# Performance work log

Measured on AMD Instinct MI355X. Metric: run time of the kernel, lower is better.

## Reference

```python
import jax, jax.numpy as jnp
import numpy as np

EMBED_DIM = 1024
NUM_HEADS = 16
NUM_KV_HEADS = 4
HEAD_DIM = 64
GQA_RATIO = NUM_HEADS // NUM_KV_HEADS
SCALE = 1.0 / np.sqrt(HEAD_DIM).astype(np.float32)
B, L = 1, 4096
NUM_SEQS = 8  # 8 packed sequences of length 512


def setup_inputs() -> dict:
    key = jax.random.key(0)
    k1, k2, k3, k4, k5 = jax.random.split(key, 5)
    hidden_states = jax.random.normal(k1, (B, L, EMBED_DIM), dtype=jnp.float32)
    cu_seqlens = (jnp.arange(NUM_SEQS + 1, dtype=jnp.int32) * (L // NUM_SEQS))
    s = 1.0 / np.sqrt(EMBED_DIM)
    Wq = jax.random.normal(k2, (EMBED_DIM, NUM_HEADS * HEAD_DIM), dtype=jnp.float32) * s
    Wk = jax.random.normal(k3, (EMBED_DIM, NUM_KV_HEADS * HEAD_DIM), dtype=jnp.float32) * s
    Wv = jax.random.normal(k4, (EMBED_DIM, NUM_KV_HEADS * HEAD_DIM), dtype=jnp.float32) * s
    Wo = jax.random.normal(k5, (NUM_HEADS * HEAD_DIM, EMBED_DIM), dtype=jnp.float32) * s
    return {"hidden_states": hidden_states, "Wq": Wq, "Wk": Wk, "Wv": Wv, "Wo": Wo,
            "cu_seqlens": cu_seqlens}


def reference(hidden_states, Wq, Wk, Wv, Wo, cu_seqlens):
    b, l, d = hidden_states.shape
    # QKV projections (Linear, no bias)
    q = (hidden_states @ Wq).reshape(b, l, NUM_HEADS, HEAD_DIM)
    k = (hidden_states @ Wk).reshape(b, l, NUM_KV_HEADS, HEAD_DIM)
    v = (hidden_states @ Wv).reshape(b, l, NUM_KV_HEADS, HEAD_DIM)
    # GQA: expand kv heads to num_heads (faithful to module's manual expand)
    k = jnp.repeat(k, GQA_RATIO, axis=2)  # [b, l, H, hd]
    v = jnp.repeat(v, GQA_RATIO, axis=2)
    # [b, H, l, hd]
    q = q.transpose(0, 2, 1, 3)
    k = k.transpose(0, 2, 1, 3)
    v = v.transpose(0, 2, 1, 3)
    # block-diagonal varlen mask from cu_seqlens
    pos = jnp.arange(l, dtype=jnp.int32)
    seq_ids = jnp.searchsorted(cu_seqlens, pos, side='right') - 1  # [l]
    mask = seq_ids[:, None] == seq_ids[None, :]                    # [l, l]
    # dense SDPA with mask
    scores = jnp.einsum('bhqd,bhkd->bhqk', q, k) * SCALE
    scores = jnp.where(mask[None, None], scores, jnp.finfo(scores.dtype).min)
    attn = jax.nn.softmax(scores, axis=-1)
    out = jnp.einsum('bhqk,bhkd->bhqd', attn, v)
    out = out.transpose(0, 2, 1, 3).reshape(b, l, NUM_HEADS * HEAD_DIM)
    return out @ Wo
```

## Files before the change

kernel.cpp:

```cpp
#include <hip/hip_runtime.h>
#include <hip/hip_bf16.h>
#include <stdint.h>
#include <stddef.h>

typedef __attribute__((ext_vector_type(8))) short short8;
typedef __attribute__((ext_vector_type(4))) short short4v;
typedef __attribute__((ext_vector_type(4))) float f32x4;

__device__ inline void store_c(float* p, float v) { *p = v; }
__device__ inline void store_c(__hip_bfloat16* p, float v) { *p = __float2bfloat16(v); }

__device__ __forceinline__ void gld_lds16(const __hip_bfloat16* g, __hip_bfloat16* l)
{
#if __has_builtin(__builtin_amdgcn_global_load_lds)
    __builtin_amdgcn_global_load_lds(
        (const __attribute__((address_space(1))) unsigned int*)g,
        (__attribute__((address_space(3))) unsigned int*)l,
        16, 0, 0);
#else
    *(short8*)((char*)l + (threadIdx.x & 63) * 16) = *(const short8*)g;
#endif
}

__global__ __launch_bounds__(256) void convert_kernel(const float* __restrict__ in,
                                                      __hip_bfloat16* __restrict__ out,
                                                      int n4)
{
    int i = blockIdx.x * blockDim.x + threadIdx.x;
    if (i >= n4) return;
    const f32x4 v = *(const f32x4*)(in + (size_t)i * 4);
    union { __hip_bfloat16 t[4]; short4v s4; } u;
    #pragma unroll
    for (int j = 0; j < 4; ++j) u.t[j] = __float2bfloat16(v[j]);
    *(short4v*)(out + (size_t)i * 4) = u.s4;
}

__global__ __launch_bounds__(256) void transpose_kernel(const float* __restrict__ Wq,
                                                        const float* __restrict__ Wk,
                                                        const float* __restrict__ Wv,
                                                        const float* __restrict__ Wo,
                                                        __hip_bfloat16* __restrict__ Wt)
{
    __shared__ float tile[32][33];
    const int bk = blockIdx.x;
    const int bn = blockIdx.y;
    const int tx = threadIdx.x & 31;
    const int ty = threadIdx.x >> 5;
    const int n0 = bn * 32;

    const float* src; int ld; int col0;
    if (n0 < 1024)      { src = Wq; ld = 1024; col0 = n0; }
    else if (n0 < 1280) { src = Wk; ld = 256;  col0 = n0 - 1024; }
    else if (n0 < 1536) { src = Wv; ld = 256;  col0 = n0 - 1280; }
    else                { src = Wo; ld = 1024; col0 = n0 - 1536; }

    #pragma unroll
    for (int r = 0; r < 4; ++r) {
        int k = ty + 8 * r;
        tile[k][tx] = src[(size_t)(bk * 32 + k) * ld + col0 + tx];
    }
    __syncthreads();
    #pragma unroll
    for (int r = 0; r < 4; ++r) {
        int nl = ty + 8 * r;
        Wt[(size_t)(n0 + nl) * 1024 + bk * 32 + tx] = __float2bfloat16(tile[tx][nl]);
    }
}

__global__ __launch_bounds__(256) void vt_kernel(const __hip_bfloat16* __restrict__ QKV,
                                                 __hip_bfloat16* __restrict__ Vt)
{
    __shared__ __hip_bfloat16 tile[32][34];
    const int j0 = blockIdx.x * 32;
    const int c0 = blockIdx.y * 32;
    const int tx = threadIdx.x & 31;
    const int ty = threadIdx.x >> 5;

    #pragma unroll
    for (int r = 0; r < 4; ++r) {
        int jl = ty + 8 * r;
        int j = j0 + jl;
        int srcrow = (j & ~63) + (j & 3) * 16 + ((j >> 2) & 15);
        tile[jl][tx] = QKV[(size_t)srcrow * 1536 + 1280 + c0 + tx];
    }
    __syncthreads();
    #pragma unroll
    for (int r = 0; r < 4; ++r) {
        int cl = ty + 8 * r;
        Vt[(size_t)(c0 + cl) * 4096 + j0 + tx] = tile[tx][cl];
    }
}

template <typename CT>
__global__ __launch_bounds__(512) void gemm128_kernel(const __hip_bfloat16* __restrict__ A,
                                                      const __hip_bfloat16* __restrict__ Bt,
                                                      CT* __restrict__ C,
                                                      int M, int N, int K)
{
    __shared__ __align__(16) __hip_bfloat16 As[128 * 64];
    __shared__ __align__(16) __hip_bfloat16 Bs[128 * 64];

    const int tid  = threadIdx.x;
    const int lane = tid & 63;
    const int wave = tid >> 6;
    const int wr = wave >> 2;
    const int wc = wave & 3;
    const int fr = lane & 15;
    const int fg = lane >> 4;

    const __hip_bfloat16* Ab = A  + (size_t)(blockIdx.x * 128) * K;
    const __hip_bfloat16* Bb = Bt + (size_t)(blockIdx.y * 128) * K;

    const int srow8 = lane >> 3;
    const int sslot = (lane & 7) ^ srow8;

    f32x4 acc[4][2];
    const f32x4 z4 = {0.f, 0.f, 0.f, 0.f};
    #pragma unroll
    for (int i = 0; i < 4; ++i)
        #pragma unroll
        for (int j = 0; j < 2; ++j) acc[i][j] = z4;

    for (int k0 = 0; k0 < K; k0 += 64) {
        #pragma unroll
        for (int i = 0; i < 2; ++i) {
            int c = wave * 2 + i;
            gld_lds16(Ab + (size_t)(c * 8 + srow8) * K + k0 + sslot * 8, &As[c * 512]);
        }
        #pragma unroll
        for (int i = 0; i < 2; ++i) {
            int c = wave * 2 + i;
            gld_lds16(Bb + (size_t)(c * 8 + srow8) * K + k0 + sslot * 8, &Bs[c * 512]);
        }
        __syncthreads();

        short8 af[2][4], bfv[2][2];
        #pragma unroll
        for (int kc = 0; kc < 2; ++kc) {
            #pragma unroll
            for (int mf = 0; mf < 4; ++mf) {
                int rr = wr * 64 + mf * 16 + fr;
                af[kc][mf] = *(const short8*)&As[rr * 64 + (((kc * 4 + fg) ^ (fr & 7)) * 8)];
            }
            #pragma unroll
            for (int nf = 0; nf < 2; ++nf) {
                int cc = wc * 32 + nf * 16 + fr;
                bfv[kc][nf] = *(const short8*)&Bs[cc * 64 + (((kc * 4 + fg) ^ (fr & 7)) * 8)];
            }
        }
        #pragma unroll
        for (int kc = 0; kc < 2; ++kc)
            #pragma unroll
            for (int mf = 0; mf < 4; ++mf)
                #pragma unroll
                for (int nf = 0; nf < 2; ++nf)
                    acc[mf][nf] = __builtin_amdgcn_mfma_f32_16x16x32_bf16(af[kc][mf], bfv[kc][nf], acc[mf][nf], 0, 0, 0);
        __syncthreads();
    }

    const int crow = blockIdx.x * 128 + wr * 64;
    const int ccol = blockIdx.y * 128 + wc * 32;
    #pragma unroll
    for (int mf = 0; mf < 4; ++mf)
        #pragma unroll
        for (int nf = 0; nf < 2; ++nf)
            #pragma unroll
            for (int r = 0; r < 4; ++r) {
                int row = crow + mf * 16 + fg * 4 + r;
                int col = ccol + nf * 16 + fr;
                store_c(&C[(size_t)row * N + col], acc[mf][nf][r]);
            }
}

__global__ __launch_bounds__(256) void attn_kernel(const __hip_bfloat16* __restrict__ QKV,
                                                   const __hip_bfloat16* __restrict__ Vt,
                                                   __hip_bfloat16* __restrict__ O)
{
    __shared__ __align__(16) __hip_bfloat16 Ks[64 * 64];
    __shared__ __align__(16) __hip_bfloat16 Vts[64 * 64];
    __shared__ __align__(16) __hip_bfloat16 Ps[4][16][72];

    const int tid  = threadIdx.x;
    const int lane = tid & 63;
    const int wave = tid >> 6;
    const int qt = blockIdx.x;
    const int h  = blockIdx.y;
    const int sq = blockIdx.z;
    const int kvh = h >> 2;

    const int fr = lane & 15;
    const int fg = lane >> 4;
    const int fk = fg * 8;

    const int sr = lane >> 3;
    const int scol = ((lane & 7) ^ sr) * 8;

    const int q0 = sq * 512 + qt * 64 + wave * 16;

    short8 qf[2];
    #pragma unroll
    for (int kc = 0; kc < 2; ++kc)
        qf[kc] = *(const short8*)(QKV + (size_t)(q0 + fr) * 1536 + h * 64 + kc * 32 + fk);

    const f32x4 z4 = {0.f, 0.f, 0.f, 0.f};
    f32x4 acc_o[4];
    #pragma unroll
    for (int b = 0; b < 4; ++b) acc_o[b] = z4;

    float m_run[4], l_run[4];
    #pragma unroll
    for (int r = 0; r < 4; ++r) { m_run[r] = -1e30f; l_run[r] = 0.f; }

    const float cs = 0.125f * 1.44269504088896340736f;

    for (int t = 0; t < 8; ++t) {
        const int kvbase = sq * 512 + t * 64;

        #pragma unroll
        for (int i = wave; i < 8; i += 4) {
            gld_lds16(QKV + (size_t)(kvbase + i * 8 + sr) * 1536 + 1024 + kvh * 64 + scol,
                      &Ks[i * 512]);
            gld_lds16(Vt + (size_t)(kvh * 64 + i * 8 + sr) * 4096 + kvbase + scol,
                      &Vts[i * 512]);
        }
        __syncthreads();

        f32x4 s[4];
        #pragma unroll
        for (int b = 0; b < 4; ++b) s[b] = z4;
        #pragma unroll
        for (int kc = 0; kc < 2; ++kc) {
            #pragma unroll
            for (int nf = 0; nf < 4; ++nf) {
                short8 kf = *(const short8*)&Ks[(nf * 16 + fr) * 64 + (((kc * 4 + fg) ^ (fr & 7)) * 8)];
                s[nf] = __builtin_amdgcn_mfma_f32_16x16x32_bf16(qf[kc], kf, s[nf], 0, 0, 0);
            }
        }

        #pragma unroll
        for (int r = 0; r < 4; ++r) {
            float mx = fmaxf(fmaxf(s[0][r], s[1][r]), fmaxf(s[2][r], s[3][r]));
            #pragma unroll
            for (int off = 1; off < 16; off <<= 1)
                mx = fmaxf(mx, __shfl_xor(mx, off));
            float mnew = fmaxf(m_run[r], mx);
            float f = exp2f((m_run[r] - mnew) * cs);
            m_run[r] = mnew;
            float p0 = exp2f((s[0][r] - mnew) * cs);
            float p1 = exp2f((s[1][r] - mnew) * cs);
            float p2 = exp2f((s[2][r] - mnew) * cs);
            float p3 = exp2f((s[3][r] - mnew) * cs);
            l_run[r] = l_run[r] * f + (p0 + p1 + p2 + p3);
            #pragma unroll
            for (int nf = 0; nf < 4; ++nf)
                acc_o[nf][r] *= f;
            int rl = fg * 4 + r;
            union { __hip_bfloat16 h[4]; short4v s4; } pw;
            pw.h[0] = __float2bfloat16(p0);
            pw.h[1] = __float2bfloat16(p1);
            pw.h[2] = __float2bfloat16(p2);
            pw.h[3] = __float2bfloat16(p3);
            *(short4v*)&Ps[wave][rl][fr * 4] = pw.s4;
        }

        #pragma unroll
        for (int kc = 0; kc < 2; ++kc) {
            short8 pa = *(const short8*)&Ps[wave][fr][kc * 32 + fk];
            #pragma unroll
            for (int nf = 0; nf < 4; ++nf) {
                short8 vf = *(const short8*)&Vts[(nf * 16 + fr) * 64 + (((kc * 4 + fg) ^ (fr & 7)) * 8)];
                acc_o[nf] = __builtin_amdgcn_mfma_f32_16x16x32_bf16(pa, vf, acc_o[nf], 0, 0, 0);
            }
        }
        __syncthreads();
    }

    #pragma unroll
    for (int r = 0; r < 4; ++r) {
        float lsum = l_run[r];
        #pragma unroll
        for (int off = 1; off < 16; off <<= 1)
            lsum += __shfl_xor(lsum, off);
        float inv_l = 1.0f / lsum;
        int row = q0 + fg * 4 + r;
        #pragma unroll
        for (int nf = 0; nf < 4; ++nf)
            O[(size_t)row * 1024 + h * 64 + nf * 16 + fr] =
                __float2bfloat16(acc_o[nf][r] * inv_l);
    }
}

extern "C" void kernel_launch(void* const* d_in, const int* in_sizes, int n_in,
                              void* d_out, int out_size, void* d_ws, size_t ws_size,
                              hipStream_t stream)
{
    const float* hs = (const float*)d_in[0];
    const float* Wq = (const float*)d_in[1];
    const float* Wk = (const float*)d_in[2];
    const float* Wv = (const float*)d_in[3];
    const float* Wo = (const float*)d_in[4];

    char* ws = (char*)d_ws;
    __hip_bfloat16* hsb  = (__hip_bfloat16*)(ws);
    __hip_bfloat16* Wt   = (__hip_bfloat16*)(ws + 8388608);
    __hip_bfloat16* QKV  = (__hip_bfloat16*)(ws + 13631488);
    __hip_bfloat16* AOut = (__hip_bfloat16*)(ws + 26214400);
    __hip_bfloat16* Vt   = (__hip_bfloat16*)(ws + 34603008);
    float* out = (float*)d_out;

    convert_kernel<<<4096, 256, 0, stream>>>(hs, hsb, 1048576);
    transpose_kernel<<<dim3(32, 80), 256, 0, stream>>>(Wq, Wk, Wv, Wo, Wt);
    gemm128_kernel<__hip_bfloat16><<<dim3(32, 12), 512, 0, stream>>>(hsb, Wt, QKV, 4096, 1536, 1024);
    vt_kernel<<<dim3(128, 8), 256, 0, stream>>>(QKV, Vt);
    attn_kernel<<<dim3(8, 16, 8), 256, 0, stream>>>(QKV, Vt, AOut);
    gemm128_kernel<float><<<dim3(32, 8), 512, 0, stream>>>(AOut, Wt + (size_t)1536 * 1024, out, 4096, 1024, 1024);
}
```

Measured before the change: 154.3 us.

## Merge convert and transpose prep kernels; retile GEMMs to 64-row blocks

Merges the fp32->bf16 activation conversion and the weight transpose into one prep kernel launch that branches on block index, saving one launch. Replaces the 128x128, 512-thread GEMM with a 64xBN, 256-thread GEMM templated on BN (192 for the QKV projection, 128 for the output projection). This gives 512 blocks per GEMM instead of 384 and 256, to fill more compute units on the MI355X. In exchange each block reuses less data per tile, so more global and LDS loads are issued per MFMA.

Result: faster. 149.4 us (-3.2%).

```diff
diff --git a/kernel.cpp b/kernel.cpp
--- a/kernel.cpp
+++ b/kernel.cpp
@@ -22,28 +22,28 @@
 #endif
 }
 
-__global__ __launch_bounds__(256) void convert_kernel(const float* __restrict__ in,
-                                                      __hip_bfloat16* __restrict__ out,
-                                                      int n4)
-{
-    int i = blockIdx.x * blockDim.x + threadIdx.x;
-    if (i >= n4) return;
-    const f32x4 v = *(const f32x4*)(in + (size_t)i * 4);
-    union { __hip_bfloat16 t[4]; short4v s4; } u;
-    #pragma unroll
-    for (int j = 0; j < 4; ++j) u.t[j] = __float2bfloat16(v[j]);
-    *(short4v*)(out + (size_t)i * 4) = u.s4;
-}
-
-__global__ __launch_bounds__(256) void transpose_kernel(const float* __restrict__ Wq,
-                                                        const float* __restrict__ Wk,
-                                                        const float* __restrict__ Wv,
-                                                        const float* __restrict__ Wo,
-                                                        __hip_bfloat16* __restrict__ Wt)
+__global__ __launch_bounds__(256) void prep_kernel(const float* __restrict__ hs,
+                                                   const float* __restrict__ Wq,
+                                                   const float* __restrict__ Wk,
+                                                   const float* __restrict__ Wv,
+                                                   const float* __restrict__ Wo,
+                                                   __hip_bfloat16* __restrict__ hsb,
+                                                   __hip_bfloat16* __restrict__ Wt)
 {
     __shared__ float tile[32][33];
-    const int bk = blockIdx.x;
-    const int bn = blockIdx.y;
+    const int b = blockIdx.x;
+    if (b < 4096) {
+        int i = b * 256 + threadIdx.x;
+        const f32x4 v = *(const f32x4*)(hs + (size_t)i * 4);
+        union { __hip_bfloat16 t[4]; short4v s4; } u;
+        #pragma unroll
+        for (int j = 0; j < 4; ++j) u.t[j] = __float2bfloat16(v[j]);
+        *(short4v*)(hsb + (size_t)i * 4) = u.s4;
+        return;
+    }
+    const int bb = b - 4096;
+    const int bk = bb & 31;
+    const int bn = bb >> 5;
     const int tx = threadIdx.x & 31;
     const int ty = threadIdx.x >> 5;
     const int n0 = bn * 32;
@@ -91,79 +91,78 @@
     }
 }
 
-template <typename CT>
-__global__ __launch_bounds__(512) void gemm128_kernel(const __hip_bfloat16* __restrict__ A,
-                                                      const __hip_bfloat16* __restrict__ Bt,
-                                                      CT* __restrict__ C,
-                                                      int M, int N, int K)
-{
-    __shared__ __align__(16) __hip_bfloat16 As[128 * 64];
-    __shared__ __align__(16) __hip_bfloat16 Bs[128 * 64];
+template <int BN, typename CT>
+__global__ __launch_bounds__(256) void gemm64_kernel(const __hip_bfloat16* __restrict__ A,
+                                                     const __hip_bfloat16* __restrict__ Bt,
+                                                     CT* __restrict__ C,
+                                                     int M, int N, int K)
+{
+    constexpr int NF = BN / 32;
+    constexpr int TC = 8 + BN / 8;
+    __shared__ __align__(16) __hip_bfloat16 As[64 * 64];
+    __shared__ __align__(16) __hip_bfloat16 Bs[BN * 64];
 
     const int tid  = threadIdx.x;
     const int lane = tid & 63;
     const int wave = tid >> 6;
-    const int wr = wave >> 2;
-    const int wc = wave & 3;
+    const int wr = wave >> 1;
+    const int wc = wave & 1;
     const int fr = lane & 15;
     const int fg = lane >> 4;
 
-    const __hip_bfloat16* Ab = A  + (size_t)(blockIdx.x * 128) * K;
-    const __hip_bfloat16* Bb = Bt + (size_t)(blockIdx.y * 128) * K;
+    const __hip_bfloat16* Ab = A  + (size_t)(blockIdx.x * 64) * K;
+    const __hip_bfloat16* Bb = Bt + (size_t)(blockIdx.y * BN) * K;
 
     const int srow8 = lane >> 3;
     const int sslot = (lane & 7) ^ srow8;
 
-    f32x4 acc[4][2];
+    f32x4 acc[2][NF];
     const f32x4 z4 = {0.f, 0.f, 0.f, 0.f};
     #pragma unroll
-    for (int i = 0; i < 4; ++i)
-        #pragma unroll
-        for (int j = 0; j < 2; ++j) acc[i][j] = z4;
+    for (int i = 0; i < 2; ++i)
+        #pragma unroll
+        for (int j = 0; j < NF; ++j) acc[i][j] = z4;
 
     for (int k0 = 0; k0 < K; k0 += 64) {
         #pragma unroll
-        for (int i = 0; i < 2; ++i) {
-            int c = wave * 2 + i;
-            gld_lds16(Ab + (size_t)(c * 8 + srow8) * K + k0 + sslot * 8, &As[c * 512]);
-        }
-        #pragma unroll
-        for (int i = 0; i < 2; ++i) {
-            int c = wave * 2 + i;
-            gld_lds16(Bb + (size_t)(c * 8 + srow8) * K + k0 + sslot * 8, &Bs[c * 512]);
+        for (int c = wave; c < TC; c += 4) {
+            if (c < 8)
+                gld_lds16(Ab + (size_t)(c * 8 + srow8) * K + k0 + sslot * 8, &As[c * 512]);
+            else
+                gld_lds16(Bb + (size_t)((c - 8) * 8 + srow8) * K + k0 + sslot * 8, &Bs[(c - 8) * 512]);
         }
         __syncthreads();
 
-        short8 af[2][4], bfv[2][2];
+        short8 af[2][2], bfv[2][NF];
         #pragma unroll
         for (int kc = 0; kc < 2; ++kc) {
             #pragma unroll
-            for (int mf = 0; mf < 4; ++mf) {
-                int rr = wr * 64 + mf * 16 + fr;
+            for (int mf = 0; mf < 2; ++mf) {
+                int rr = wr * 32 + mf * 16 + fr;
                 af[kc][mf] = *(const short8*)&As[rr * 64 + (((kc * 4 + fg) ^ (fr & 7)) * 8)];
             }
             #pragma unroll
-            for (int nf = 0; nf < 2; ++nf) {
-                int cc = wc * 32 + nf * 16 + fr;
+            for (int nf = 0; nf < NF; ++nf) {
+                int cc = wc * (BN / 2) + nf * 16 + fr;
                 bfv[kc][nf] = *(const short8*)&Bs[cc * 64 + (((kc * 4 + fg) ^ (fr & 7)) * 8)];
             }
         }
         #pragma unroll
         for (int kc = 0; kc < 2; ++kc)
             #pragma unroll
-            for (int mf = 0; mf < 4; ++mf)
+            for (int mf = 0; mf < 2; ++mf)
                 #pragma unroll
-                for (int nf = 0; nf < 2; ++nf)
+                for (int nf = 0; nf < NF; ++nf)
                     acc[mf][nf] = __builtin_amdgcn_mfma_f32_16x16x32_bf16(af[kc][mf], bfv[kc][nf], acc[mf][nf], 0, 0, 0);
         __syncthreads();
     }
 
-    const int crow = blockIdx.x * 128 + wr * 64;
-    const int ccol = blockIdx.y * 128 + wc * 32;
-    #pragma unroll
-    for (int mf = 0; mf < 4; ++mf)
-        #pragma unroll
-        for (int nf = 0; nf < 2; ++nf)
+    const int crow = blockIdx.x * 64 + wr * 32;
+    const int ccol = blockIdx.y * BN + wc * (BN / 2);
+    #pragma unroll
+    for (int mf = 0; mf < 2; ++mf)
+        #pragma unroll
+        for (int nf = 0; nf < NF; ++nf)
             #pragma unroll
             for (int r = 0; r < 4; ++r) {
                 int row = crow + mf * 16 + fg * 4 + r;
@@ -308,10 +307,9 @@
     __hip_bfloat16* Vt   = (__hip_bfloat16*)(ws + 34603008);
     float* out = (float*)d_out;
 
-    convert_kernel<<<4096, 256, 0, stream>>>(hs, hsb, 1048576);
-    transpose_kernel<<<dim3(32, 80), 256, 0, stream>>>(Wq, Wk, Wv, Wo, Wt);
-    gemm128_kernel<__hip_bfloat16><<<dim3(32, 12), 512, 0, stream>>>(hsb, Wt, QKV, 4096, 1536, 1024);
+    prep_kernel<<<6656, 256, 0, stream>>>(hs, Wq, Wk, Wv, Wo, hsb, Wt);
+    gemm64_kernel<192, __hip_bfloat16><<<dim3(64, 8), 256, 0, stream>>>(hsb, Wt, QKV, 4096, 1536, 1024);
     vt_kernel<<<dim3(128, 8), 256, 0, stream>>>(QKV, Vt);
     attn_kernel<<<dim3(8, 16, 8), 256, 0, stream>>>(QKV, Vt, AOut);
-    gemm128_kernel<float><<<dim3(32, 8), 512, 0, stream>>>(AOut, Wt + (size_t)1536 * 1024, out, 4096, 1024, 1024);
-}
+    gemm64_kernel<128, float><<<dim3(64, 8), 256, 0, stream>>>(AOut, Wt + (size_t)1536 * 1024, out, 4096, 1024, 1024);
+}
```
